# Optimization experiments

Hardware: AMD Instinct MI355X
Metric: run time of the kernel (lower is better)

## Reference

```python
import jax, jax.numpy as jnp
import numpy as np

B, N, D, H, DEG = 2, 20000, 256, 8, 8
E = N * DEG
EPS = 1e-3  # keras LayerNormalization default epsilon


def layer_norm(x, gamma, beta):
    mu = jnp.mean(x, axis=-1, keepdims=True)
    var = jnp.mean(jnp.square(x - mu), axis=-1, keepdims=True)
    return (x - mu) * jax.lax.rsqrt(var + EPS) * gamma + beta


def setup_inputs() -> dict:
    key = jax.random.key(0)
    ks = jax.random.split(key, 8)
    x = jax.random.normal(ks[0], (B, N, D), dtype=jnp.float32)
    # edge list sorted by source node; every node has DEG out-edges so
    # segment_sum covers all N segments (matches tf.math.segment_sum semantics)
    src = jnp.repeat(jnp.arange(N, dtype=jnp.int64), DEG)
    dst = jax.random.randint(ks[1], (E,), 0, N, dtype=jnp.int64)
    edges = jnp.stack([src, dst], axis=1)  # [E, 2]
    scale = 0.05
    wq = jax.random.normal(ks[2], (D, D), dtype=jnp.float32) * scale
    wk = jax.random.normal(ks[3], (D, D), dtype=jnp.float32) * scale
    wv = jax.random.normal(ks[4], (D, D), dtype=jnp.float32) * scale
    wo = jax.random.normal(ks[5], (D, D), dtype=jnp.float32) * scale
    zeros = jnp.zeros((D,), dtype=jnp.float32)
    ones = jnp.ones((D,), dtype=jnp.float32)
    return {
        "x": x, "edges": edges,
        "wq": wq, "bq": zeros, "wk": wk, "bk": zeros,
        "wv": wv, "bv": zeros, "wo": wo, "bo": zeros,
        "gamma1": ones, "beta1": zeros, "gamma2": ones, "beta2": zeros,
    }


def reference(x, edges, wq, bq, wk, bk, wv, bv, wo, bo, gamma1, beta1, gamma2, beta2):
    b, n, d = x.shape
    h, dh = H, D // H
    xn = layer_norm(x, gamma1, beta1)                      # [B,N,D]
    # QKV projections, split heads, move node axis to front: [N,B,H,dh]
    def proj(w, bias):
        y = (xn @ w + bias).reshape(b, n, h, dh)
        return jnp.transpose(y, (1, 0, 2, 3))
    q, k, v = proj(wq, bq), proj(wk, bk), proj(wv, bv)
    src, dst = edges[:, 0], edges[:, 1]
    q_part = q[src]                                         # [E,B,H,dh]
    k_part = k[dst]
    v_part = v[dst]
    logits = jnp.sum(q_part * k_part, axis=-1, keepdims=True) / jnp.sqrt(
        jnp.asarray(dh, dtype=x.dtype))                     # [E,B,H,1]
    w = jnp.exp(logits)                                     # unnormalized softmax (as in source)
    num = jax.ops.segment_sum(v_part * w, src, num_segments=n)  # [N,B,H,dh]
    den = jax.ops.segment_sum(w, src, num_segments=n)           # [N,B,H,1]
    attn = num / den
    attn = jnp.transpose(attn, (1, 0, 2, 3)).reshape(b, n, d)   # [B,N,D]
    concat = xn + attn                                      # residual uses normed input (source reassigns `inputs`)
    out = layer_norm(concat, gamma2, beta2)
    out = jax.nn.relu(out @ wo + bo)
    return out + concat
```

## Files before the change

### kernel.cpp

```cpp
#include <hip/hip_runtime.h>


typedef __bf16 bf16x8 __attribute__((ext_vector_type(8)));
typedef float  f32x4  __attribute__((ext_vector_type(4)));

__device__ __forceinline__ float bf2f(unsigned short u) {
    union { unsigned int i; float f; } v; v.i = ((unsigned int)u) << 16; return v.f;
}
__device__ __forceinline__ unsigned short f2bf(float f) {
    union { float f; unsigned int i; } v; v.f = f;
    unsigned int x = v.i;
    unsigned int r = (x + 0x7FFFu + ((x >> 16) & 1u)) >> 16;
    return (unsigned short)r;
}

#define NNODE 20000
#define ROWS  40000
#define DMODEL 256

__global__ __launch_bounds__(256) void prep_ln1_kernel(
    const float* __restrict__ wq, const float* __restrict__ wk,
    const float* __restrict__ wv, const float* __restrict__ wo,
    const float* __restrict__ bq, const float* __restrict__ bk,
    const float* __restrict__ bv, const float* __restrict__ bo,
    const float* __restrict__ x,
    const float* __restrict__ g1, const float* __restrict__ b1,
    unsigned short* __restrict__ Wqkvt,
    unsigned short* __restrict__ Wot,
    float* __restrict__ biasq,
    float* __restrict__ biaso,
    unsigned short* __restrict__ xn)
{
    if (blockIdx.x < 1024) {
        int idx = blockIdx.x * 256 + threadIdx.x;
        if (idx < 768 * 256) {
            int n = idx >> 8, k = idx & 255;
            int sel = n >> 8, nl = n & 255;
            const float* w = (sel == 0) ? wq : (sel == 1) ? wk : wv;
            Wqkvt[idx] = f2bf(w[k * 256 + nl]);
        } else {
            int idx2 = idx - 768 * 256;
            int n = idx2 >> 8, k = idx2 & 255;
            Wot[idx2] = f2bf(wo[k * 256 + n]);
        }
        if (idx < 768) {
            const float* bb = (idx < 256) ? bq : (idx < 512) ? bk : bv;
            biasq[idx] = bb[idx & 255];
        }
        if (idx >= 768 && idx < 1024) biaso[idx - 768] = bo[idx - 768];
        return;
    }
    int wave = threadIdx.x >> 6, lane = threadIdx.x & 63;
    int sub = lane >> 5, hl = lane & 31;
    int m = (blockIdx.x - 1024) * 8 + wave * 2 + sub;
    const float* xp = x + (size_t)m * DMODEL + hl * 8;
    float4 x0 = *(const float4*)xp;
    float4 x1 = *(const float4*)(xp + 4);
    float f[8] = {x0.x, x0.y, x0.z, x0.w, x1.x, x1.y, x1.z, x1.w};
    float s = 0.f, ss = 0.f;
    #pragma unroll
    for (int t = 0; t < 8; ++t) { s += f[t]; ss += f[t]*f[t]; }
    #pragma unroll
    for (int mk = 1; mk < 32; mk <<= 1) { s += __shfl_xor(s, mk); ss += __shfl_xor(ss, mk); }
    float mu  = s * (1.f/256.f);
    float var = ss * (1.f/256.f) - mu*mu;
    float rs  = rsqrtf(var + 1e-3f);
    float4 g0 = *(const float4*)(g1 + hl * 8);
    float4 g1v = *(const float4*)(g1 + hl * 8 + 4);
    float4 b0 = *(const float4*)(b1 + hl * 8);
    float4 b1v = *(const float4*)(b1 + hl * 8 + 4);
    float gg[8] = {g0.x, g0.y, g0.z, g0.w, g1v.x, g1v.y, g1v.z, g1v.w};
    float bb[8] = {b0.x, b0.y, b0.z, b0.w, b1v.x, b1v.y, b1v.z, b1v.w};
    unsigned short o[8];
    #pragma unroll
    for (int t = 0; t < 8; ++t) o[t] = f2bf((f[t] - mu) * rs * gg[t] + bb[t]);
    *(int4*)(xn + (size_t)m * DMODEL + hl * 8) = *(const int4*)o;
}

#define LDS_W 72
#define MFMA_BF16(d, a, b) d = __builtin_amdgcn_mfma_f32_16x16x32_bf16(a, b, d, 0, 0, 0)

template<bool EPI>
__global__ __launch_bounds__(256, 2) void gemm_kernel(
    const unsigned short* __restrict__ A,
    const unsigned short* __restrict__ Bt,
    const float* __restrict__ bias,
    void* __restrict__ C,
    const unsigned short* __restrict__ resid,
    int M, int Ncols)
{
    __shared__ unsigned short As[128 * LDS_W];
    __shared__ unsigned short Bs[128 * LDS_W];
    int tid  = threadIdx.x;
    int wave = tid >> 6, lane = tid & 63;
    int quad = lane >> 4, l16 = lane & 15;
    int m0 = blockIdx.x * 128, n0 = blockIdx.y * 128;
    int wm = (wave >> 1) * 64, wn = (wave & 1) * 64;

    int srow = tid >> 1;
    int sseg = (tid & 1) * 32;
    int arow = m0 + srow; if (arow >= M) arow = M - 1;
    const unsigned short* ArowP = A  + (size_t)arow * 256 + sseg;
    const unsigned short* BrowP = Bt + (size_t)(n0 + srow) * 256 + sseg;
    unsigned short* AsP = &As[srow * LDS_W + sseg];
    unsigned short* BsP = &Bs[srow * LDS_W + sseg];

    f32x4 acc00 = {}, acc01 = {}, acc02 = {}, acc03 = {};
    f32x4 acc10 = {}, acc11 = {}, acc12 = {}, acc13 = {};
    f32x4 acc20 = {}, acc21 = {}, acc22 = {}, acc23 = {};
    f32x4 acc30 = {}, acc31 = {}, acc32 = {}, acc33 = {};

    for (int kt = 0; kt < 4; ++kt) {
        const unsigned short* ap = ArowP + kt * 64;
        const unsigned short* bp = BrowP + kt * 64;
        int4 va0 = *(const int4*)(ap);
        int4 va1 = *(const int4*)(ap + 8);
        int4 va2 = *(const int4*)(ap + 16);
        int4 va3 = *(const int4*)(ap + 24);
        int4 vb0 = *(const int4*)(bp);
        int4 vb1 = *(const int4*)(bp + 8);
        int4 vb2 = *(const int4*)(bp + 16);
        int4 vb3 = *(const int4*)(bp + 24);
        __syncthreads();
        *(int4*)(AsP)      = va0;
        *(int4*)(AsP + 8)  = va1;
        *(int4*)(AsP + 16) = va2;
        *(int4*)(AsP + 24) = va3;
        *(int4*)(BsP)      = vb0;
        *(int4*)(BsP + 8)  = vb1;
        *(int4*)(BsP + 16) = vb2;
        *(int4*)(BsP + 24) = vb3;
        __syncthreads();
        #pragma unroll
        for (int ks = 0; ks < 64; ks += 32) {
            bf16x8 a0 = *(const bf16x8*)&As[(wm +  0 + l16) * LDS_W + ks + quad * 8];
            bf16x8 a1 = *(const bf16x8*)&As[(wm + 16 + l16) * LDS_W + ks + quad * 8];
            bf16x8 a2 = *(const bf16x8*)&As[(wm + 32 + l16) * LDS_W + ks + quad * 8];
            bf16x8 a3 = *(const bf16x8*)&As[(wm + 48 + l16) * LDS_W + ks + quad * 8];
            bf16x8 b0 = *(const bf16x8*)&Bs[(wn +  0 + l16) * LDS_W + ks + quad * 8];
            bf16x8 b1 = *(const bf16x8*)&Bs[(wn + 16 + l16) * LDS_W + ks + quad * 8];
            bf16x8 b2 = *(const bf16x8*)&Bs[(wn + 32 + l16) * LDS_W + ks + quad * 8];
            bf16x8 b3 = *(const bf16x8*)&Bs[(wn + 48 + l16) * LDS_W + ks + quad * 8];
            MFMA_BF16(acc00, a0, b0); MFMA_BF16(acc01, a0, b1);
            MFMA_BF16(acc02, a0, b2); MFMA_BF16(acc03, a0, b3);
            MFMA_BF16(acc10, a1, b0); MFMA_BF16(acc11, a1, b1);
            MFMA_BF16(acc12, a1, b2); MFMA_BF16(acc13, a1, b3);
            MFMA_BF16(acc20, a2, b0); MFMA_BF16(acc21, a2, b1);
            MFMA_BF16(acc22, a2, b2); MFMA_BF16(acc23, a2, b3);
            MFMA_BF16(acc30, a3, b0); MFMA_BF16(acc31, a3, b1);
            MFMA_BF16(acc32, a3, b2); MFMA_BF16(acc33, a3, b3);
        }
    }

#define EPI_STORE(accv, R, CC) do {                                          \
        int col = n0 + wn + (CC) * 16 + l16;                                 \
        float bb = bias[col];                                                \
        int rowb = m0 + wm + (R) * 16 + quad * 4;                            \
        _Pragma("unroll")                                                    \
        for (int rr = 0; rr < 4; ++rr) {                                     \
            int row = rowb + rr;                                             \
            if (row < M) {                                                   \
                float v = (accv)[rr] + bb;                                   \
                if (EPI) {                                                   \
                    v = fmaxf(v, 0.f);                                       \
                    v += bf2f(resid[(size_t)row * 256 + col]);               \
                    ((float*)C)[(size_t)row * Ncols + col] = v;              \
                } else {                                                     \
                    ((unsigned short*)C)[(size_t)row * Ncols + col] = f2bf(v);\
                }                                                            \
            }                                                                \
        }                                                                    \
    } while (0)

    EPI_STORE(acc00, 0, 0); EPI_STORE(acc01, 0, 1); EPI_STORE(acc02, 0, 2); EPI_STORE(acc03, 0, 3);
    EPI_STORE(acc10, 1, 0); EPI_STORE(acc11, 1, 1); EPI_STORE(acc12, 1, 2); EPI_STORE(acc13, 1, 3);
    EPI_STORE(acc20, 2, 0); EPI_STORE(acc21, 2, 1); EPI_STORE(acc22, 2, 2); EPI_STORE(acc23, 2, 3);
    EPI_STORE(acc30, 3, 0); EPI_STORE(acc31, 3, 1); EPI_STORE(acc32, 3, 2); EPI_STORE(acc33, 3, 3);
#undef EPI_STORE
}

__global__ __launch_bounds__(256) void attn_kernel(
    const unsigned short* __restrict__ qkv,
    const int* __restrict__ edges,
    const unsigned short* __restrict__ xn,
    const float* __restrict__ g2, const float* __restrict__ b2,
    unsigned short* __restrict__ concat,
    unsigned short* __restrict__ h2)
{
    int wave = threadIdx.x >> 6, lane = threadIdx.x & 63;
    int i = blockIdx.x * 4 + wave;
    int b = lane >> 5, hl = lane & 31;
    size_t m = (size_t)b * NNODE + i;

    int4 qi = *(const int4*)(qkv + m * 768 + hl * 8);
    const unsigned short* qs = (const unsigned short*)&qi;
    float qf[8];
    #pragma unroll
    for (int t = 0; t < 8; ++t) qf[t] = bf2f(qs[t]);

    int jv = 0;
    if (lane < 8) jv = edges[2 * (i * 8 + lane) + 1];

#define KVLOAD(E)                                                                  \
    int j##E = __shfl(jv, E);                                                      \
    const unsigned short* kp##E = qkv + ((size_t)b * NNODE + j##E) * 768 + 256 + hl * 8; \
    int4 KI##E = *(const int4*)(kp##E);                                            \
    int4 VI##E = *(const int4*)(kp##E + 256);
    KVLOAD(0) KVLOAD(1) KVLOAD(2) KVLOAD(3)
    KVLOAD(4) KVLOAD(5) KVLOAD(6) KVLOAD(7)
#undef KVLOAD

    float acc[8] = {};
    float den = 0.f;
    const float scale = 0.17677669529663687f;
#define EDGE(E) do {                                                         \
        const unsigned short* ks = (const unsigned short*)&KI##E;            \
        const unsigned short* vs = (const unsigned short*)&VI##E;            \
        float dot = 0.f;                                                     \
        _Pragma("unroll")                                                    \
        for (int t = 0; t < 8; ++t) dot += qf[t] * bf2f(ks[t]);              \
        dot += __shfl_xor(dot, 1);                                           \
        dot += __shfl_xor(dot, 2);               \
        float w = __expf(dot * scale);                                       \
        _Pragma("unroll")                                                    \
        for (int t = 0; t < 8; ++t) acc[t] += w * bf2f(vs[t]);               \
        den += w;                                                            \
    } while (0)
    EDGE(0); EDGE(1); EDGE(2); EDGE(3);
    EDGE(4); EDGE(5); EDGE(6); EDGE(7);
#undef EDGE
    float inv = 1.f / den;

    int4 xi = *(const int4*)(xn + m * DMODEL + hl * 8);
    const unsigned short* xs = (const unsigned short*)&xi;
    float c[8], s = 0.f, ss = 0.f;
    #pragma unroll
    for (int t = 0; t < 8; ++t) { c[t] = bf2f(xs[t]) + acc[t] * inv; s += c[t]; ss += c[t]*c[t]; }
    #pragma unroll
    for (int mk = 1; mk < 32; mk <<= 1) { s += __shfl_xor(s, mk); ss += __shfl_xor(ss, mk); }
    float mu  = s * (1.f/256.f);
    float var = ss * (1.f/256.f) - mu*mu;
    float rs  = rsqrtf(var + 1e-3f);

    float4 ga = *(const float4*)(g2 + hl * 8);
    float4 gb = *(const float4*)(g2 + hl * 8 + 4);
    float4 ba = *(const float4*)(b2 + hl * 8);
    float4 bb = *(const float4*)(b2 + hl * 8 + 4);
    float gg[8] = {ga.x, ga.y, ga.z, ga.w, gb.x, gb.y, gb.z, gb.w};
    float bv[8] = {ba.x, ba.y, ba.z, ba.w, bb.x, bb.y, bb.z, bb.w};
    unsigned short oc[8], oh[8];
    #pragma unroll
    for (int t = 0; t < 8; ++t) {
        oc[t] = f2bf(c[t]);
        oh[t] = f2bf((c[t] - mu) * rs * gg[t] + bv[t]);
    }
    *(int4*)(concat + m * DMODEL + hl * 8) = *(const int4*)oc;
    *(int4*)(h2     + m * DMODEL + hl * 8) = *(const int4*)oh;
}

extern "C" void kernel_launch(void* const* d_in, const int* in_sizes, int n_in,
                              void* d_out, int out_size, void* d_ws, size_t ws_size,
                              hipStream_t stream)
{
    const float* x   = (const float*)d_in[0];
    const int* edges = (const int*)d_in[1];
    const float* wq = (const float*)d_in[2];
    const float* bq = (const float*)d_in[3];
    const float* wk = (const float*)d_in[4];
    const float* bk = (const float*)d_in[5];
    const float* wv = (const float*)d_in[6];
    const float* bv = (const float*)d_in[7];
    const float* wo = (const float*)d_in[8];
    const float* bo = (const float*)d_in[9];
    const float* g1 = (const float*)d_in[10];
    const float* b1 = (const float*)d_in[11];
    const float* g2 = (const float*)d_in[12];
    const float* b2 = (const float*)d_in[13];

    char* ws = (char*)d_ws;
    unsigned short* Wqkvt = (unsigned short*)(ws);
    unsigned short* Wot   = (unsigned short*)(ws + 393216);
    float* biasq          = (float*)(ws + 393216 + 131072);
    float* biaso          = (float*)(ws + 393216 + 131072 + 3072);
    size_t off = 393216 + 131072 + 4096;
    unsigned short* xn     = (unsigned short*)(ws + off); off += (size_t)ROWS * DMODEL * 2;
    unsigned short* qkv    = (unsigned short*)(ws + off); off += (size_t)ROWS * 768 * 2;
    unsigned short* concat = (unsigned short*)(ws + off); off += (size_t)ROWS * DMODEL * 2;
    unsigned short* h2     = (unsigned short*)(ws + off); off += (size_t)ROWS * DMODEL * 2;

    prep_ln1_kernel<<<1024 + ROWS / 8, 256, 0, stream>>>(
        wq, wk, wv, wo, bq, bk, bv, bo, x, g1, b1, Wqkvt, Wot, biasq, biaso, xn);
    gemm_kernel<false><<<dim3(313, 6), 256, 0, stream>>>(xn, Wqkvt, biasq, qkv, nullptr, ROWS, 768);
    attn_kernel<<<NNODE / 4, 256, 0, stream>>>(qkv, edges, xn, g2, b2, concat, h2);
    gemm_kernel<true><<<dim3(313, 2), 256, 0, stream>>>(h2, Wot, biaso, d_out, concat, ROWS, 256);
}
```

Before: 235.6 us.

## Prefetch next GEMM k-tile into registers and remap blocks per XCD

The GEMM now loads the next 64-wide k-slice from global memory into registers while the current slice's MFMAs run, so global latency overlaps with compute. It also switches to a 1D grid with an XCD-aware block remap, so consecutive tiles sharing A rows land on the same XCD and reuse its L2. In the attention kernel the xn load is hoisted to the start so it overlaps with the gathers. The cost is higher register pressure from the prefetch registers, which may affect occupancy at 2 blocks per CU.

```diff
diff --git a/kernel.cpp b/kernel.cpp
--- a/kernel.cpp
+++ b/kernel.cpp
@@ -94,7 +94,16 @@
     int tid  = threadIdx.x;
     int wave = tid >> 6, lane = tid & 63;
     int quad = lane >> 4, l16 = lane & 15;
-    int m0 = blockIdx.x * 128, n0 = blockIdx.y * 128;
+
+    int nt_total = Ncols >> 7;
+    int nwg = gridDim.x;
+    int xcd = blockIdx.x & 7, loc = blockIdx.x >> 3;
+    int qq = nwg >> 3, rr = nwg & 7;
+    int wid = (xcd < rr) ? (xcd * (qq + 1) + loc)
+                         : (rr * (qq + 1) + (xcd - rr) * qq + loc);
+    int mt = wid / nt_total;
+    int nt = wid - mt * nt_total;
+    int m0 = mt * 128, n0 = nt * 128;
     int wm = (wave >> 1) * 64, wn = (wave & 1) * 64;
 
     int srow = tid >> 1;
@@ -110,17 +119,16 @@
     f32x4 acc20 = {}, acc21 = {}, acc22 = {}, acc23 = {};
     f32x4 acc30 = {}, acc31 = {}, acc32 = {}, acc33 = {};
 
+    int4 va0 = *(const int4*)(ArowP);
+    int4 va1 = *(const int4*)(ArowP + 8);
+    int4 va2 = *(const int4*)(ArowP + 16);
+    int4 va3 = *(const int4*)(ArowP + 24);
+    int4 vb0 = *(const int4*)(BrowP);
+    int4 vb1 = *(const int4*)(BrowP + 8);
+    int4 vb2 = *(const int4*)(BrowP + 16);
+    int4 vb3 = *(const int4*)(BrowP + 24);
+
     for (int kt = 0; kt < 4; ++kt) {
-        const unsigned short* ap = ArowP + kt * 64;
-        const unsigned short* bp = BrowP + kt * 64;
-        int4 va0 = *(const int4*)(ap);
-        int4 va1 = *(const int4*)(ap + 8);
-        int4 va2 = *(const int4*)(ap + 16);
-        int4 va3 = *(const int4*)(ap + 24);
-        int4 vb0 = *(const int4*)(bp);
-        int4 vb1 = *(const int4*)(bp + 8);
-        int4 vb2 = *(const int4*)(bp + 16);
-        int4 vb3 = *(const int4*)(bp + 24);
         __syncthreads();
         *(int4*)(AsP)      = va0;
         *(int4*)(AsP + 8)  = va1;
@@ -131,6 +139,18 @@
         *(int4*)(BsP + 16) = vb2;
         *(int4*)(BsP + 24) = vb3;
         __syncthreads();
+        if (kt < 3) {
+            const unsigned short* ap = ArowP + (kt + 1) * 64;
+            const unsigned short* bp = BrowP + (kt + 1) * 64;
+            va0 = *(const int4*)(ap);
+            va1 = *(const int4*)(ap + 8);
+            va2 = *(const int4*)(ap + 16);
+            va3 = *(const int4*)(ap + 24);
+            vb0 = *(const int4*)(bp);
+            vb1 = *(const int4*)(bp + 8);
+            vb2 = *(const int4*)(bp + 16);
+            vb3 = *(const int4*)(bp + 24);
+        }
         #pragma unroll
         for (int ks = 0; ks < 64; ks += 32) {
             bf16x8 a0 = *(const bf16x8*)&As[(wm +  0 + l16) * LDS_W + ks + quad * 8];
@@ -193,6 +213,7 @@
     size_t m = (size_t)b * NNODE + i;
 
     int4 qi = *(const int4*)(qkv + m * 768 + hl * 8);
+    int4 xi = *(const int4*)(xn + m * DMODEL + hl * 8);
     const unsigned short* qs = (const unsigned short*)&qi;
     float qf[8];
     #pragma unroll
@@ -231,7 +252,6 @@
 #undef EDGE
     float inv = 1.f / den;
 
-    int4 xi = *(const int4*)(xn + m * DMODEL + hl * 8);
     const unsigned short* xs = (const unsigned short*)&xi;
     float c[8], s = 0.f, ss = 0.f;
     #pragma unroll
@@ -290,7 +310,7 @@
 
     prep_ln1_kernel<<<1024 + ROWS / 8, 256, 0, stream>>>(
         wq, wk, wv, wo, bq, bk, bv, bo, x, g1, b1, Wqkvt, Wot, biasq, biaso, xn);
-    gemm_kernel<false><<<dim3(313, 6), 256, 0, stream>>>(xn, Wqkvt, biasq, qkv, nullptr, ROWS, 768);
+    gemm_kernel<false><<<dim3(313 * 6), 256, 0, stream>>>(xn, Wqkvt, biasq, qkv, nullptr, ROWS, 768);
     attn_kernel<<<NNODE / 4, 256, 0, stream>>>(qkv, edges, xn, g2, b2, concat, h2);
-    gemm_kernel<true><<<dim3(313, 2), 256, 0, stream>>>(h2, Wot, biaso, d_out, concat, ROWS, 256);
-}
+    gemm_kernel<true><<<dim3(313 * 2), 256, 0, stream>>>(h2, Wot, biaso, d_out, concat, ROWS, 256);
+}
```

New measurement: 228.9 us. -2.8%, faster.
